# Kernel tuning notes

Hardware: AMD Instinct MI355X
Metric: run time of the kernel (lower is better)

## Reference

```python
import jax, jax.numpy as jnp
import numpy as np

N_NODES = 50000
N_EDGES = 600000
F_DIM = 128


def setup_inputs() -> dict:
    key = jax.random.key(0)
    k_x, k_e, k_w1, k_b1, k_w2, k_b2 = jax.random.split(key, 6)
    x = jax.random.normal(k_x, (N_NODES, F_DIM), dtype=jnp.float32)
    edge_index = jax.random.randint(k_e, (2, N_EDGES), 0, N_NODES, dtype=jnp.int64)
    # nn.Linear-style params (weight is [out, in])
    s1 = 1.0 / np.sqrt(F_DIM)
    w1 = jax.random.uniform(k_w1, (128, F_DIM), jnp.float32, -s1, s1)
    b1 = jax.random.uniform(k_b1, (128,), jnp.float32, -s1, s1)
    s2 = 1.0 / np.sqrt(128)
    w2 = jax.random.uniform(k_w2, (F_DIM, 128), jnp.float32, -s2, s2)
    b2 = jax.random.uniform(k_b2, (F_DIM,), jnp.float32, -s2, s2)
    return {"x": x, "edge_index": edge_index, "w1": w1, "b1": b1, "w2": w2, "b2": b2}


def reference(x, edge_index, w1, b1, w2, b2):
    n = x.shape[0]
    # add_self_loops: append (i, i) for every node
    loops = jnp.arange(n, dtype=edge_index.dtype)
    src = jnp.concatenate([edge_index[0], loops])  # [E + N]
    dst = jnp.concatenate([edge_index[1], loops])  # [E + N]

    def conv(h):
        h = h @ w1.T + b1          # [N, 128]
        h = h @ w2.T + b2          # [N, F]
        msgs = h[src]              # gather source features [E+N, F]
        return jax.ops.segment_sum(msgs, dst, num_segments=n)  # scatter-add

    h = conv(conv(x))
    return jax.nn.log_softmax(h, axis=1)
```

## Files before the change

### kernel.cpp

```cpp
#include <hip/hip_runtime.h>
#include <hip/hip_bf16.h>

#define N_NODES 50000
#define N_EDGES 600000
#define F 128
#define BCAP 64

typedef unsigned short bf16_t;
typedef __attribute__((ext_vector_type(8))) short short8v;
typedef __attribute__((ext_vector_type(8))) unsigned short ushort8v;
typedef __attribute__((ext_vector_type(4))) float f32x4;

__device__ inline float bf2f(bf16_t u) {
    union { unsigned int i; float f; } c;
    c.i = ((unsigned int)u) << 16;
    return c.f;
}
__device__ inline bf16_t f2bf(float f) {
    union { float f; unsigned int i; } c;
    c.f = f;
    unsigned int lsb = (c.i >> 16) & 1;
    c.i += 0x7fffu + lsb;
    return (bf16_t)(c.i >> 16);
}

__global__ void k_fuse(const float* __restrict__ w1, const float* __restrict__ b1,
                       const float* __restrict__ w2, const float* __restrict__ b2,
                       float* __restrict__ Wc, float* __restrict__ bc,
                       int* __restrict__ cnt) {
    int p = blockIdx.x;
    int j = threadIdx.x;
    int gid = p * 128 + j;
    for (int i = gid; i < N_NODES; i += 128 * 128) cnt[i] = 0;

    float s = 0.f;
    for (int o = 0; o < F; ++o) s = fmaf(w2[p * F + o], w1[o * F + j], s);
    Wc[p * F + j] = s;
    if (j == 0) {
        float t = b2[p];
        for (int o = 0; o < F; ++o) t = fmaf(w2[p * F + o], b1[o], t);
        bc[p] = t;
    }
}

__global__ void k_fuse2(const float* __restrict__ Wc, const float* __restrict__ bc,
                        bf16_t* __restrict__ Mbf, float* __restrict__ v1) {
    int k = blockIdx.x;
    int p = threadIdx.x;
    float s = 0.f;
    for (int o = 0; o < F; ++o) s = fmaf(Wc[p * F + o], Wc[o * F + k], s);
    Mbf[p * F + k] = f2bf(s);
    if (k == 0) {
        float t = 0.f;
        for (int o = 0; o < F; ++o) t = fmaf(Wc[p * F + o], bc[o], t);
        v1[p] = t;
    }
}

__global__ __launch_bounds__(256)
void k_fill(const int* __restrict__ src, const int* __restrict__ dst,
            int* __restrict__ cnt, int* __restrict__ bucket) {
    int e = blockIdx.x * 256 + threadIdx.x;
    if (e >= N_EDGES) return;
    int d = dst[e];
    int slot = atomicAdd(&cnt[d], 1);
    if (slot < BCAP) bucket[d * BCAP + slot] = src[e];
}

__global__ __launch_bounds__(256, 2)
void k_gemm_mfma(const float* __restrict__ X, const bf16_t* __restrict__ Mbf,
                 bf16_t* __restrict__ G, int n_rows) {
    extern __shared__ unsigned short smem[];
    unsigned short* Xs = smem;
    unsigned short* Ms = smem + 8192;
    const int tid = threadIdx.x;
    const int row0 = blockIdx.x * 64;

    for (int idx = tid; idx < 2048; idx += 256) {
        int p = idx >> 4, c = idx & 15;
        ushort8v v = ((const ushort8v*)Mbf)[idx];
        *(ushort8v*)&Ms[p * 128 + (((c ^ (p & 7)) << 3))] = v;
    }
    for (int idx = tid; idx < 1024; idx += 256) {
        int r = idx >> 4, c = idx & 15;
        int grow = row0 + r;
        float4 va = {0.f, 0.f, 0.f, 0.f}, vb = {0.f, 0.f, 0.f, 0.f};
        if (grow < n_rows) {
            const float4* xr = (const float4*)(X + (size_t)grow * F);
            va = xr[2 * c];
            vb = xr[2 * c + 1];
        }
        ushort8v u;
        u[0] = f2bf(va.x); u[1] = f2bf(va.y); u[2] = f2bf(va.z); u[3] = f2bf(va.w);
        u[4] = f2bf(vb.x); u[5] = f2bf(vb.y); u[6] = f2bf(vb.z); u[7] = f2bf(vb.w);
        *(ushort8v*)&Xs[r * 128 + (((c ^ (r & 7)) << 3))] = u;
    }
    __syncthreads();

    const int wid = tid >> 6;
    const int lane = tid & 63;
    const int wr = wid >> 1;
    const int wc = wid & 1;
    const int l15 = lane & 15;
    const int l4 = lane >> 4;
    const int sw = (l15 & 7);

    f32x4 acc[2][4] = {};

#pragma unroll
    for (int kc = 0; kc < 4; ++kc) {
        const int cS = ((kc * 4 + l4) ^ sw) << 3;
        short8v a0 = *(const short8v*)&Xs[(wr * 32 + 0 * 16 + l15) * 128 + cS];
        short8v a1 = *(const short8v*)&Xs[(wr * 32 + 1 * 16 + l15) * 128 + cS];
        short8v b0 = *(const short8v*)&Ms[(wc * 64 + 0 * 16 + l15) * 128 + cS];
        short8v b1 = *(const short8v*)&Ms[(wc * 64 + 1 * 16 + l15) * 128 + cS];
        short8v b2 = *(const short8v*)&Ms[(wc * 64 + 2 * 16 + l15) * 128 + cS];
        short8v b3 = *(const short8v*)&Ms[(wc * 64 + 3 * 16 + l15) * 128 + cS];
        acc[0][0] = __builtin_amdgcn_mfma_f32_16x16x32_bf16(a0, b0, acc[0][0], 0, 0, 0);
        acc[0][1] = __builtin_amdgcn_mfma_f32_16x16x32_bf16(a0, b1, acc[0][1], 0, 0, 0);
        acc[0][2] = __builtin_amdgcn_mfma_f32_16x16x32_bf16(a0, b2, acc[0][2], 0, 0, 0);
        acc[0][3] = __builtin_amdgcn_mfma_f32_16x16x32_bf16(a0, b3, acc[0][3], 0, 0, 0);
        acc[1][0] = __builtin_amdgcn_mfma_f32_16x16x32_bf16(a1, b0, acc[1][0], 0, 0, 0);
        acc[1][1] = __builtin_amdgcn_mfma_f32_16x16x32_bf16(a1, b1, acc[1][1], 0, 0, 0);
        acc[1][2] = __builtin_amdgcn_mfma_f32_16x16x32_bf16(a1, b2, acc[1][2], 0, 0, 0);
        acc[1][3] = __builtin_amdgcn_mfma_f32_16x16x32_bf16(a1, b3, acc[1][3], 0, 0, 0);
    }

#pragma unroll
    for (int mt = 0; mt < 2; ++mt) {
#pragma unroll
        for (int nt = 0; nt < 4; ++nt) {
#pragma unroll
            for (int r = 0; r < 4; ++r) {
                int grow = row0 + wr * 32 + mt * 16 + l4 * 4 + r;
                if (grow < n_rows) {
                    int gcol = wc * 64 + nt * 16 + l15;
                    G[(size_t)grow * F + gcol] = f2bf(acc[mt][nt][r]);
                }
            }
        }
    }
}

__global__ __launch_bounds__(256)
void k_agg(const bf16_t* __restrict__ H, const int* __restrict__ cnt,
           const int* __restrict__ bucket, bf16_t* __restrict__ O, int n_rows) {
    int tid = threadIdx.x;
    int lane = tid & 31;
    int node = blockIdx.x * 8 + (tid >> 5);
    if (node >= n_rows) return;

    int deg = cnt[node];
    if (deg > BCAP) deg = BCAP;
    ushort4 u = ((const ushort4*)(H + (size_t)node * F))[lane];
    float a0 = bf2f(u.x), a1 = bf2f(u.y), a2 = bf2f(u.z), a3 = bf2f(u.w);

    const int* bk = bucket + node * BCAP;
    int i = 0;
    for (; i + 8 <= deg; i += 8) {
        int4 s4 = *(const int4*)(bk + i);
        int4 s5 = *(const int4*)(bk + i + 4);
        ushort4 u0 = ((const ushort4*)(H + (size_t)s4.x * F))[lane];
        ushort4 u1 = ((const ushort4*)(H + (size_t)s4.y * F))[lane];
        ushort4 u2 = ((const ushort4*)(H + (size_t)s4.z * F))[lane];
        ushort4 u3 = ((const ushort4*)(H + (size_t)s4.w * F))[lane];
        ushort4 u4 = ((const ushort4*)(H + (size_t)s5.x * F))[lane];
        ushort4 u5 = ((const ushort4*)(H + (size_t)s5.y * F))[lane];
        ushort4 u6 = ((const ushort4*)(H + (size_t)s5.z * F))[lane];
        ushort4 u7 = ((const ushort4*)(H + (size_t)s5.w * F))[lane];
        a0 += bf2f(u0.x) + bf2f(u1.x) + bf2f(u2.x) + bf2f(u3.x)
            + bf2f(u4.x) + bf2f(u5.x) + bf2f(u6.x) + bf2f(u7.x);
        a1 += bf2f(u0.y) + bf2f(u1.y) + bf2f(u2.y) + bf2f(u3.y)
            + bf2f(u4.y) + bf2f(u5.y) + bf2f(u6.y) + bf2f(u7.y);
        a2 += bf2f(u0.z) + bf2f(u1.z) + bf2f(u2.z) + bf2f(u3.z)
            + bf2f(u4.z) + bf2f(u5.z) + bf2f(u6.z) + bf2f(u7.z);
        a3 += bf2f(u0.w) + bf2f(u1.w) + bf2f(u2.w) + bf2f(u3.w)
            + bf2f(u4.w) + bf2f(u5.w) + bf2f(u6.w) + bf2f(u7.w);
    }
    for (; i + 4 <= deg; i += 4) {
        int4 s4 = *(const int4*)(bk + i);
        ushort4 u0 = ((const ushort4*)(H + (size_t)s4.x * F))[lane];
        ushort4 u1 = ((const ushort4*)(H + (size_t)s4.y * F))[lane];
        ushort4 u2 = ((const ushort4*)(H + (size_t)s4.z * F))[lane];
        ushort4 u3 = ((const ushort4*)(H + (size_t)s4.w * F))[lane];
        a0 += bf2f(u0.x) + bf2f(u1.x) + bf2f(u2.x) + bf2f(u3.x);
        a1 += bf2f(u0.y) + bf2f(u1.y) + bf2f(u2.y) + bf2f(u3.y);
        a2 += bf2f(u0.z) + bf2f(u1.z) + bf2f(u2.z) + bf2f(u3.z);
        a3 += bf2f(u0.w) + bf2f(u1.w) + bf2f(u2.w) + bf2f(u3.w);
    }
    for (; i < deg; ++i) {
        ushort4 uv = ((const ushort4*)(H + (size_t)bk[i] * F))[lane];
        a0 += bf2f(uv.x); a1 += bf2f(uv.y); a2 += bf2f(uv.z); a3 += bf2f(uv.w);
    }
    ushort4 o;
    o.x = f2bf(a0); o.y = f2bf(a1); o.z = f2bf(a2); o.w = f2bf(a3);
    ((ushort4*)(O + (size_t)node * F))[lane] = o;
}

__global__ __launch_bounds__(256)
void k_agg_ep(const bf16_t* __restrict__ H, const int* __restrict__ cnt,
              const int* __restrict__ bucket,
              const float* __restrict__ v1, const float* __restrict__ bc,
              float* __restrict__ O, int n_rows) {
    int tid = threadIdx.x;
    int lane = tid & 31;
    int node = blockIdx.x * 8 + (tid >> 5);
    if (node >= n_rows) return;

    int deg_t = cnt[node];
    int deg = deg_t < BCAP ? deg_t : BCAP;
    ushort4 u = ((const ushort4*)(H + (size_t)node * F))[lane];
    float a0 = bf2f(u.x), a1 = bf2f(u.y), a2 = bf2f(u.z), a3 = bf2f(u.w);

    const int* bk = bucket + node * BCAP;

    int sdi = (lane == 0) ? (deg_t + 1) : 0;
    for (int j = lane; j < deg; j += 32) sdi += cnt[bk[j]] + 1;

    int i = 0;
    for (; i + 8 <= deg; i += 8) {
        int4 s4 = *(const int4*)(bk + i);
        int4 s5 = *(const int4*)(bk + i + 4);
        ushort4 u0 = ((const ushort4*)(H + (size_t)s4.x * F))[lane];
        ushort4 u1 = ((const ushort4*)(H + (size_t)s4.y * F))[lane];
        ushort4 u2 = ((const ushort4*)(H + (size_t)s4.z * F))[lane];
        ushort4 u3 = ((const ushort4*)(H + (size_t)s4.w * F))[lane];
        ushort4 u4 = ((const ushort4*)(H + (size_t)s5.x * F))[lane];
        ushort4 u5 = ((const ushort4*)(H + (size_t)s5.y * F))[lane];
        ushort4 u6 = ((const ushort4*)(H + (size_t)s5.z * F))[lane];
        ushort4 u7 = ((const ushort4*)(H + (size_t)s5.w * F))[lane];
        a0 += bf2f(u0.x) + bf2f(u1.x) + bf2f(u2.x) + bf2f(u3.x)
            + bf2f(u4.x) + bf2f(u5.x) + bf2f(u6.x) + bf2f(u7.x);
        a1 += bf2f(u0.y) + bf2f(u1.y) + bf2f(u2.y) + bf2f(u3.y)
            + bf2f(u4.y) + bf2f(u5.y) + bf2f(u6.y) + bf2f(u7.y);
        a2 += bf2f(u0.z) + bf2f(u1.z) + bf2f(u2.z) + bf2f(u3.z)
            + bf2f(u4.z) + bf2f(u5.z) + bf2f(u6.z) + bf2f(u7.z);
        a3 += bf2f(u0.w) + bf2f(u1.w) + bf2f(u2.w) + bf2f(u3.w)
            + bf2f(u4.w) + bf2f(u5.w) + bf2f(u6.w) + bf2f(u7.w);
    }
    for (; i + 4 <= deg; i += 4) {
        int4 s4 = *(const int4*)(bk + i);
        ushort4 u0 = ((const ushort4*)(H + (size_t)s4.x * F))[lane];
        ushort4 u1 = ((const ushort4*)(H + (size_t)s4.y * F))[lane];
        ushort4 u2 = ((const ushort4*)(H + (size_t)s4.z * F))[lane];
        ushort4 u3 = ((const ushort4*)(H + (size_t)s4.w * F))[lane];
        a0 += bf2f(u0.x) + bf2f(u1.x) + bf2f(u2.x) + bf2f(u3.x);
        a1 += bf2f(u0.y) + bf2f(u1.y) + bf2f(u2.y) + bf2f(u3.y);
        a2 += bf2f(u0.z) + bf2f(u1.z) + bf2f(u2.z) + bf2f(u3.z);
        a3 += bf2f(u0.w) + bf2f(u1.w) + bf2f(u2.w) + bf2f(u3.w);
    }
    for (; i < deg; ++i) {
        ushort4 uv = ((const ushort4*)(H + (size_t)bk[i] * F))[lane];
        a0 += bf2f(uv.x); a1 += bf2f(uv.y); a2 += bf2f(uv.z); a3 += bf2f(uv.w);
    }

#pragma unroll
    for (int o = 16; o; o >>= 1) sdi += __shfl_xor(sdi, o);
    float sdn = (float)sdi;
    float dn = (float)(deg_t + 1);
    float4 v1v = ((const float4*)v1)[lane];
    float4 bcv = ((const float4*)bc)[lane];
    a0 += sdn * v1v.x + dn * bcv.x;
    a1 += sdn * v1v.y + dn * bcv.y;
    a2 += sdn * v1v.z + dn * bcv.z;
    a3 += sdn * v1v.w + dn * bcv.w;

    float m = fmaxf(fmaxf(a0, a1), fmaxf(a2, a3));
#pragma unroll
    for (int o = 16; o; o >>= 1) m = fmaxf(m, __shfl_xor(m, o));
    float s = expf(a0 - m) + expf(a1 - m) + expf(a2 - m) + expf(a3 - m);
#pragma unroll
    for (int o = 16; o; o >>= 1) s += __shfl_xor(s, o);
    float lse = m + logf(s);
    float4 o4;
    o4.x = a0 - lse; o4.y = a1 - lse; o4.z = a2 - lse; o4.w = a3 - lse;
    ((float4*)(O + (size_t)node * F))[lane] = o4;
}

extern "C" void kernel_launch(void* const* d_in, const int* in_sizes, int n_in,
                              void* d_out, int out_size, void* d_ws, size_t ws_size,
                              hipStream_t stream) {
    const float* x  = (const float*)d_in[0];
    const int* ei   = (const int*)d_in[1];
    const float* w1 = (const float*)d_in[2];
    const float* b1 = (const float*)d_in[3];
    const float* w2 = (const float*)d_in[4];
    const float* b2 = (const float*)d_in[5];
    float* out = (float*)d_out;

    const int* src = ei;
    const int* dst = ei + N_EDGES;

    float* ws     = (float*)d_ws;
    float* Wc     = ws;
    float* bc     = ws + 16384;
    float* v1     = ws + 16512;
    bf16_t* Mbf   = (bf16_t*)(ws + 16640);
    int*   cnt    = (int*)(ws + 24832);
    int*   bucket = (int*)(ws + 74880);
    bf16_t* g     = (bf16_t*)(ws + 3274880);
    bf16_t* a1    = (bf16_t*)(ws + 6474880);

    const int gemm_grid = (N_NODES + 63) / 64;
    const size_t gemm_lds = (64 + 128) * 128 * sizeof(bf16_t);
    const int fill_grid = (N_EDGES + 255) / 256;
    const int node_grid = (N_NODES + 7) / 8;

    k_fuse<<<128, 128, 0, stream>>>(w1, b1, w2, b2, Wc, bc, cnt);
    k_fuse2<<<128, 128, 0, stream>>>(Wc, bc, Mbf, v1);
    k_fill<<<fill_grid, 256, 0, stream>>>(src, dst, cnt, bucket);

    k_gemm_mfma<<<gemm_grid, 256, gemm_lds, stream>>>(x, Mbf, g, N_NODES);
    k_agg<<<node_grid, 256, 0, stream>>>(g, cnt, bucket, a1, N_NODES);
    k_agg_ep<<<node_grid, 256, 0, stream>>>(a1, cnt, bucket, v1, bc, out, N_NODES);
}
```

Baseline: 126.8 us.

## Fuse edge bucketing into GEMM launch, use 16-bit bucket indices, read weights from global

Merges the edge-fill kernel and the MFMA GEMM into a single launch, with the leading blocks doing the GEMM and the trailing blocks doing atomic bucket fills, so the two independent phases overlap and one launch is saved. Bucket source indices are stored as unsigned short, which halves index traffic in the aggregation kernels. The GEMM no longer stages the weight matrix in LDS and reads B fragments straight from global memory, which cuts LDS use and allows higher occupancy. Node ids up to 50000 fit in 16 bits, so the narrowing holds for this problem size but caps the node count.

```diff
diff --git a/kernel.cpp b/kernel.cpp
--- a/kernel.cpp
+++ b/kernel.cpp
@@ -5,6 +5,9 @@
 #define N_EDGES 600000
 #define F 128
 #define BCAP 64
+
+#define GEMM_BLOCKS 782
+#define FILL_BLOCKS 2344
 
 typedef unsigned short bf16_t;
 typedef __attribute__((ext_vector_type(8))) short short8v;
@@ -57,35 +60,32 @@
     }
 }
 
-__global__ __launch_bounds__(256)
-void k_fill(const int* __restrict__ src, const int* __restrict__ dst,
-            int* __restrict__ cnt, int* __restrict__ bucket) {
-    int e = blockIdx.x * 256 + threadIdx.x;
-    if (e >= N_EDGES) return;
-    int d = dst[e];
-    int slot = atomicAdd(&cnt[d], 1);
-    if (slot < BCAP) bucket[d * BCAP + slot] = src[e];
-}
-
-__global__ __launch_bounds__(256, 2)
-void k_gemm_mfma(const float* __restrict__ X, const bf16_t* __restrict__ Mbf,
-                 bf16_t* __restrict__ G, int n_rows) {
-    extern __shared__ unsigned short smem[];
-    unsigned short* Xs = smem;
-    unsigned short* Ms = smem + 8192;
+__global__ __launch_bounds__(256, 4)
+void k_main(const float* __restrict__ X, const bf16_t* __restrict__ Mbf,
+            bf16_t* __restrict__ G,
+            const int* __restrict__ src, const int* __restrict__ dst,
+            int* __restrict__ cnt, unsigned short* __restrict__ bucket) {
+    const int bid = blockIdx.x;
     const int tid = threadIdx.x;
-    const int row0 = blockIdx.x * 64;
-
-    for (int idx = tid; idx < 2048; idx += 256) {
-        int p = idx >> 4, c = idx & 15;
-        ushort8v v = ((const ushort8v*)Mbf)[idx];
-        *(ushort8v*)&Ms[p * 128 + (((c ^ (p & 7)) << 3))] = v;
-    }
+
+    if (bid >= GEMM_BLOCKS) {
+        int e = (bid - GEMM_BLOCKS) * 256 + tid;
+        if (e < N_EDGES) {
+            int d = dst[e];
+            int slot = atomicAdd(&cnt[d], 1);
+            if (slot < BCAP) bucket[d * BCAP + slot] = (unsigned short)src[e];
+        }
+        return;
+    }
+
+    __shared__ unsigned short Xs[64 * 128];
+    const int row0 = bid * 64;
+
     for (int idx = tid; idx < 1024; idx += 256) {
         int r = idx >> 4, c = idx & 15;
         int grow = row0 + r;
         float4 va = {0.f, 0.f, 0.f, 0.f}, vb = {0.f, 0.f, 0.f, 0.f};
-        if (grow < n_rows) {
+        if (grow < N_NODES) {
             const float4* xr = (const float4*)(X + (size_t)grow * F);
             va = xr[2 * c];
             vb = xr[2 * c + 1];
@@ -112,10 +112,11 @@
         const int cS = ((kc * 4 + l4) ^ sw) << 3;
         short8v a0 = *(const short8v*)&Xs[(wr * 32 + 0 * 16 + l15) * 128 + cS];
         short8v a1 = *(const short8v*)&Xs[(wr * 32 + 1 * 16 + l15) * 128 + cS];
-        short8v b0 = *(const short8v*)&Ms[(wc * 64 + 0 * 16 + l15) * 128 + cS];
-        short8v b1 = *(const short8v*)&Ms[(wc * 64 + 1 * 16 + l15) * 128 + cS];
-        short8v b2 = *(const short8v*)&Ms[(wc * 64 + 2 * 16 + l15) * 128 + cS];
-        short8v b3 = *(const short8v*)&Ms[(wc * 64 + 3 * 16 + l15) * 128 + cS];
+        const bf16_t* mb = Mbf + (size_t)(wc * 64 + l15) * F + kc * 32 + 8 * l4;
+        short8v b0 = *(const short8v*)(mb + 0 * 16 * F);
+        short8v b1 = *(const short8v*)(mb + 1 * 16 * F);
+        short8v b2 = *(const short8v*)(mb + 2 * 16 * F);
+        short8v b3 = *(const short8v*)(mb + 3 * 16 * F);
         acc[0][0] = __builtin_amdgcn_mfma_f32_16x16x32_bf16(a0, b0, acc[0][0], 0, 0, 0);
         acc[0][1] = __builtin_amdgcn_mfma_f32_16x16x32_bf16(a0, b1, acc[0][1], 0, 0, 0);
         acc[0][2] = __builtin_amdgcn_mfma_f32_16x16x32_bf16(a0, b2, acc[0][2], 0, 0, 0);
@@ -133,7 +134,7 @@
 #pragma unroll
             for (int r = 0; r < 4; ++r) {
                 int grow = row0 + wr * 32 + mt * 16 + l4 * 4 + r;
-                if (grow < n_rows) {
+                if (grow < N_NODES) {
                     int gcol = wc * 64 + nt * 16 + l15;
                     G[(size_t)grow * F + gcol] = f2bf(acc[mt][nt][r]);
                 }
@@ -144,7 +145,8 @@
 
 __global__ __launch_bounds__(256)
 void k_agg(const bf16_t* __restrict__ H, const int* __restrict__ cnt,
-           const int* __restrict__ bucket, bf16_t* __restrict__ O, int n_rows) {
+           const unsigned short* __restrict__ bucket, bf16_t* __restrict__ O,
+           int n_rows) {
     int tid = threadIdx.x;
     int lane = tid & 31;
     int node = blockIdx.x * 8 + (tid >> 5);
@@ -155,19 +157,18 @@
     ushort4 u = ((const ushort4*)(H + (size_t)node * F))[lane];
     float a0 = bf2f(u.x), a1 = bf2f(u.y), a2 = bf2f(u.z), a3 = bf2f(u.w);
 
-    const int* bk = bucket + node * BCAP;
+    const unsigned short* bk = bucket + node * BCAP;
     int i = 0;
     for (; i + 8 <= deg; i += 8) {
-        int4 s4 = *(const int4*)(bk + i);
-        int4 s5 = *(const int4*)(bk + i + 4);
-        ushort4 u0 = ((const ushort4*)(H + (size_t)s4.x * F))[lane];
-        ushort4 u1 = ((const ushort4*)(H + (size_t)s4.y * F))[lane];
-        ushort4 u2 = ((const ushort4*)(H + (size_t)s4.z * F))[lane];
-        ushort4 u3 = ((const ushort4*)(H + (size_t)s4.w * F))[lane];
-        ushort4 u4 = ((const ushort4*)(H + (size_t)s5.x * F))[lane];
-        ushort4 u5 = ((const ushort4*)(H + (size_t)s5.y * F))[lane];
-        ushort4 u6 = ((const ushort4*)(H + (size_t)s5.z * F))[lane];
-        ushort4 u7 = ((const ushort4*)(H + (size_t)s5.w * F))[lane];
+        ushort8v s8 = *(const ushort8v*)(bk + i);
+        ushort4 u0 = ((const ushort4*)(H + (size_t)s8[0] * F))[lane];
+        ushort4 u1 = ((const ushort4*)(H + (size_t)s8[1] * F))[lane];
+        ushort4 u2 = ((const ushort4*)(H + (size_t)s8[2] * F))[lane];
+        ushort4 u3 = ((const ushort4*)(H + (size_t)s8[3] * F))[lane];
+        ushort4 u4 = ((const ushort4*)(H + (size_t)s8[4] * F))[lane];
+        ushort4 u5 = ((const ushort4*)(H + (size_t)s8[5] * F))[lane];
+        ushort4 u6 = ((const ushort4*)(H + (size_t)s8[6] * F))[lane];
+        ushort4 u7 = ((const ushort4*)(H + (size_t)s8[7] * F))[lane];
         a0 += bf2f(u0.x) + bf2f(u1.x) + bf2f(u2.x) + bf2f(u3.x)
             + bf2f(u4.x) + bf2f(u5.x) + bf2f(u6.x) + bf2f(u7.x);
         a1 += bf2f(u0.y) + bf2f(u1.y) + bf2f(u2.y) + bf2f(u3.y)
@@ -178,7 +179,7 @@
             + bf2f(u4.w) + bf2f(u5.w) + bf2f(u6.w) + bf2f(u7.w);
     }
     for (; i + 4 <= deg; i += 4) {
-        int4 s4 = *(const int4*)(bk + i);
+        ushort4 s4 = *(const ushort4*)(bk + i);
         ushort4 u0 = ((const ushort4*)(H + (size_t)s4.x * F))[lane];
         ushort4 u1 = ((const ushort4*)(H + (size_t)s4.y * F))[lane];
         ushort4 u2 = ((const ushort4*)(H + (size_t)s4.z * F))[lane];
@@ -199,7 +200,7 @@
 
 __global__ __launch_bounds__(256)
 void k_agg_ep(const bf16_t* __restrict__ H, const int* __restrict__ cnt,
-              const int* __restrict__ bucket,
+              const unsigned short* __restrict__ bucket,
               const float* __restrict__ v1, const float* __restrict__ bc,
               float* __restrict__ O, int n_rows) {
     int tid = threadIdx.x;
@@ -212,23 +213,22 @@
     ushort4 u = ((const ushort4*)(H + (size_t)node * F))[lane];
     float a0 = bf2f(u.x), a1 = bf2f(u.y), a2 = bf2f(u.z), a3 = bf2f(u.w);
 
-    const int* bk = bucket + node * BCAP;
+    const unsigned short* bk = bucket + node * BCAP;
 
     int sdi = (lane == 0) ? (deg_t + 1) : 0;
     for (int j = lane; j < deg; j += 32) sdi += cnt[bk[j]] + 1;
 
     int i = 0;
     for (; i + 8 <= deg; i += 8) {
-        int4 s4 = *(const int4*)(bk + i);
-        int4 s5 = *(const int4*)(bk + i + 4);
-        ushort4 u0 = ((const ushort4*)(H + (size_t)s4.x * F))[lane];
-        ushort4 u1 = ((const ushort4*)(H + (size_t)s4.y * F))[lane];
-        ushort4 u2 = ((const ushort4*)(H + (size_t)s4.z * F))[lane];
-        ushort4 u3 = ((const ushort4*)(H + (size_t)s4.w * F))[lane];
-        ushort4 u4 = ((const ushort4*)(H + (size_t)s5.x * F))[lane];
-        ushort4 u5 = ((const ushort4*)(H + (size_t)s5.y * F))[lane];
-        ushort4 u6 = ((const ushort4*)(H + (size_t)s5.z * F))[lane];
-        ushort4 u7 = ((const ushort4*)(H + (size_t)s5.w * F))[lane];
+        ushort8v s8 = *(const ushort8v*)(bk + i);
+        ushort4 u0 = ((const ushort4*)(H + (size_t)s8[0] * F))[lane];
+        ushort4 u1 = ((const ushort4*)(H + (size_t)s8[1] * F))[lane];
+        ushort4 u2 = ((const ushort4*)(H + (size_t)s8[2] * F))[lane];
+        ushort4 u3 = ((const ushort4*)(H + (size_t)s8[3] * F))[lane];
+        ushort4 u4 = ((const ushort4*)(H + (size_t)s8[4] * F))[lane];
+        ushort4 u5 = ((const ushort4*)(H + (size_t)s8[5] * F))[lane];
+        ushort4 u6 = ((const ushort4*)(H + (size_t)s8[6] * F))[lane];
+        ushort4 u7 = ((const ushort4*)(H + (size_t)s8[7] * F))[lane];
         a0 += bf2f(u0.x) + bf2f(u1.x) + bf2f(u2.x) + bf2f(u3.x)
             + bf2f(u4.x) + bf2f(u5.x) + bf2f(u6.x) + bf2f(u7.x);
         a1 += bf2f(u0.y) + bf2f(u1.y) + bf2f(u2.y) + bf2f(u3.y)
@@ -239,7 +239,7 @@
             + bf2f(u4.w) + bf2f(u5.w) + bf2f(u6.w) + bf2f(u7.w);
     }
     for (; i + 4 <= deg; i += 4) {
-        int4 s4 = *(const int4*)(bk + i);
+        ushort4 s4 = *(const ushort4*)(bk + i);
         ushort4 u0 = ((const ushort4*)(H + (size_t)s4.x * F))[lane];
         ushort4 u1 = ((const ushort4*)(H + (size_t)s4.y * F))[lane];
         ushort4 u2 = ((const ushort4*)(H + (size_t)s4.z * F))[lane];
@@ -291,26 +291,23 @@
     const int* src = ei;
     const int* dst = ei + N_EDGES;
 
-    float* ws     = (float*)d_ws;
-    float* Wc     = ws;
-    float* bc     = ws + 16384;
-    float* v1     = ws + 16512;
-    bf16_t* Mbf   = (bf16_t*)(ws + 16640);
-    int*   cnt    = (int*)(ws + 24832);
-    int*   bucket = (int*)(ws + 74880);
-    bf16_t* g     = (bf16_t*)(ws + 3274880);
-    bf16_t* a1    = (bf16_t*)(ws + 6474880);
-
-    const int gemm_grid = (N_NODES + 63) / 64;
-    const size_t gemm_lds = (64 + 128) * 128 * sizeof(bf16_t);
-    const int fill_grid = (N_EDGES + 255) / 256;
+    float* ws        = (float*)d_ws;
+    float* Wc        = ws;
+    float* bc        = ws + 16384;
+    float* v1        = ws + 16512;
+    bf16_t* Mbf      = (bf16_t*)(ws + 16640);
+    int*   cnt       = (int*)(ws + 24832);
+    unsigned short* bucket = (unsigned short*)(ws + 74880);
+    bf16_t* g        = (bf16_t*)(ws + 1674880);
+    bf16_t* a1       = (bf16_t*)(ws + 4874880);
+
     const int node_grid = (N_NODES + 7) / 8;
 
     k_fuse<<<128, 128, 0, stream>>>(w1, b1, w2, b2, Wc, bc, cnt);
     k_fuse2<<<128, 128, 0, stream>>>(Wc, bc, Mbf, v1);
-    k_fill<<<fill_grid, 256, 0, stream>>>(src, dst, cnt, bucket);
-
-    k_gemm_mfma<<<gemm_grid, 256, gemm_lds, stream>>>(x, Mbf, g, N_NODES);
+
+    k_main<<<GEMM_BLOCKS + FILL_BLOCKS, 256, 0, stream>>>(x, Mbf, g, src, dst,
+                                                          cnt, bucket);
     k_agg<<<node_grid, 256, 0, stream>>>(g, cnt, bucket, a1, N_NODES);
     k_agg_ep<<<node_grid, 256, 0, stream>>>(a1, cnt, bucket, v1, bc, out, N_NODES);
 }
```

Result: faster. 121.1 us (-4.5%).
